# Kernel tuning notes

Measured on AMD Instinct MI355X. Metric: run time of the kernel, lower is better.

The kernel has to match this reference:

```python
import jax, jax.numpy as jnp
import numpy as np

B, N, H, T = 4096, 512, 1024, 10  # batch, input_size, hidden_size, num_iterations
NUM_OPS = 20


def setup_inputs() -> dict:
    key = jax.random.key(0)
    k1, k2, k3, k4 = jax.random.split(key, 4)
    return {
        "x": jax.random.normal(k1, (B, N, 1), jnp.float32),
        "frozen_weight": jax.random.normal(k2, (1, N, H), jnp.float32) / np.sqrt(H),
        "alpha": jax.random.normal(k3, (T, NUM_OPS), jnp.float32),
        "layer_beta": jax.random.normal(k4, (T, 2), jnp.float32),
    }


def _softshrink(x, lam):
    return jnp.where(x > lam, x - lam, jnp.where(x < -lam, x + lam, jnp.zeros_like(x)))


def _hardshrink(x, lam):
    return jnp.where(jnp.abs(x) > lam, x, jnp.zeros_like(x))


def _make_ops(lam):
    # Same 20 ops, same order as the torch ModuleList.
    return [
        lambda x: _softshrink(x, lam),                 # Softshrink(0.001/L)
        jax.nn.relu,                                   # ReLU
        lambda x: x,                                   # Identity
        lambda x: jax.nn.gelu(x, approximate=False),   # GELU (exact erf, torch default)
        jax.nn.elu,                                    # ELU
        lambda x: _hardshrink(x, lam),                 # Hardshrink(0.001/L)
        lambda x: jnp.clip(x, -1.0, 1.0),              # Hardtanh
        jax.nn.hard_swish,                             # Hardswish
        jax.nn.selu,                                   # SELU
        jax.nn.celu,                                   # CELU
        jax.nn.leaky_relu,                             # LeakyReLU (slope 0.01)
        jax.nn.log_sigmoid,                            # LogSigmoid
        lambda x: x - jnp.tanh(x),                     # Tanhshrink
        jax.nn.soft_sign,                              # Softsign
        jax.nn.softplus,                               # Softplus
        jnp.tanh,                                      # Tanh
        jax.nn.sigmoid,                                # Sigmoid
        jax.nn.hard_sigmoid,                           # Hardsigmoid
        jax.nn.silu,                                   # SiLU
        lambda x: x * jnp.tanh(jax.nn.softplus(x)),    # Mish
    ]


def _forward(x, frozen_weight, alpha, layer_beta):
    W = frozen_weight[0]                       # [N, H]
    L = jnp.linalg.norm(W, ord=2) ** 2         # spectral norm squared (Lipschitz)
    lam = 0.001 / L
    ops = _make_ops(lam)

    b = x.shape[0]
    hidden = W.shape[1]
    z = jnp.zeros((b, hidden, 1), dtype=x.dtype)
    z_prev = z
    num_iters = alpha.shape[0]
    for i in range(num_iters):
        aw = jax.nn.softmax(alpha[i])          # [20] (training path, eval_flag=False)
        bw = jax.nn.softmax(layer_beta[i])     # [2]
        # FISTA-style momentum + frozen-weight gradient step
        z_aux = z + (i / (i + 3)) * (z - z_prev)      # [B,H,1]
        Wz = jnp.einsum('nh,bho->bno', W, z_aux)      # [B,N,1]
        grad = jnp.einsum('nh,bno->bho', W, Wz - x)   # [B,H,1]
        z_g = z_aux - grad / L
        # 20-way weighted activation mixture
        z_op = aw[0] * ops[0](z_g)
        for w, op in zip(aw[1:], ops[1:]):
            z_op = z_op + w * op(z_g)
        # beta-weighted residual mix becomes z_prev; z_op becomes current_z
        z_prev = z * bw[0] + z_op * bw[1]
        z = z_op
    return z


def reference(x, frozen_weight, alpha, layer_beta):
    return _forward(x, frozen_weight, alpha, layer_beta)
```

## Files before the change

kernel.cpp:

```cpp
#include <hip/hip_runtime.h>
#include <hip/hip_bf16.h>

#define DI __device__ __forceinline__

typedef float f32x4 __attribute__((ext_vector_type(4)));
typedef __bf16 bf16x8 __attribute__((ext_vector_type(8)));
using bf16_t = __hip_bfloat16;
using ushort_t = unsigned short;

DI void gload_lds16(const void* g, void* l) {
  __builtin_amdgcn_global_load_lds(
      (const __attribute__((address_space(1))) void*)g,
      (__attribute__((address_space(3))) void*)l, 16, 0, 0);
}

DI float rcpf(float x) { return __builtin_amdgcn_rcpf(x); }

DI float act_mix(float x, const float* aw, float lam) {
  const float ax  = fabsf(x);
  const float en  = __expf(-ax);
  const float en2 = en * en;
  const float i1  = rcpf(1.0f + en);
  const float sig = (x >= 0.0f) ? i1 : en * i1;
  const float th  = copysignf((1.0f - en2) * rcpf(1.0f + en2), x);
  const float l1p = __logf(1.0f + en);
  const float sp  = fmaxf(x, 0.0f) + l1p;
  const float lsg = fminf(x, 0.0f) - l1p;
  const float q   = ((x >= 0.0f) ? en2 : 1.0f) * (i1 * i1);
  const float mish = x * (1.0f - q) * rcpf(1.0f + q);
  const float u  = 0.7071067811865476f * x;
  const float au = fabsf(u);
  const float t  = rcpf(1.0f + 0.3275911f * au);
  float poly = fmaf(t, 1.061405429f, -1.453152027f);
  poly = fmaf(t, poly, 1.421413741f);
  poly = fmaf(t, poly, -0.284496736f);
  poly = fmaf(t, poly, 0.254829592f);
  poly *= t;
  const float erfa = 1.0f - poly * __expf(-u * u);
  const float gelu = 0.5f * x * (1.0f + copysignf(erfa, x));
  const float em1  = en - 1.0f;
  const float elu  = (x > 0.0f) ? x : em1;
  const float selu = (x > 0.0f) ? 1.0507009873554805f * x : 1.7580993408473766f * em1;
  const float relu = fmaxf(x, 0.0f);
  const float t6   = fminf(fmaxf(x + 3.0f, 0.0f), 6.0f) * 0.16666666666666666f;
  const float ssh  = (x > lam) ? (x - lam) : ((x < -lam) ? (x + lam) : 0.0f);
  const float hsh  = (ax > lam) ? x : 0.0f;
  const float htan = fminf(fmaxf(x, -1.0f), 1.0f);
  const float lky  = (x >= 0.0f) ? x : 0.01f * x;
  const float ssn  = x * rcpf(1.0f + ax);
  float r = aw[0] * ssh;
  r = fmaf(aw[1],  relu,   r);
  r = fmaf(aw[2],  x,      r);
  r = fmaf(aw[3],  gelu,   r);
  r = fmaf(aw[4],  elu,    r);
  r = fmaf(aw[5],  hsh,    r);
  r = fmaf(aw[6],  htan,   r);
  r = fmaf(aw[7],  x * t6, r);
  r = fmaf(aw[8],  selu,   r);
  r = fmaf(aw[9],  elu,    r);
  r = fmaf(aw[10], lky,    r);
  r = fmaf(aw[11], lsg,    r);
  r = fmaf(aw[12], x - th, r);
  r = fmaf(aw[13], ssn,    r);
  r = fmaf(aw[14], sp,     r);
  r = fmaf(aw[15], th,     r);
  r = fmaf(aw[16], sig,    r);
  r = fmaf(aw[17], t6,     r);
  r = fmaf(aw[18], x * sig, r);
  r = fmaf(aw[19], mish,   r);
  return r;
}

__global__ void k_prep(const float* __restrict__ W, const float* __restrict__ x,
                       bf16_t* __restrict__ Whi, bf16_t* __restrict__ Wlo,
                       bf16_t* __restrict__ Wth, bf16_t* __restrict__ Wtl,
                       bf16_t* __restrict__ xb) {
  int i = blockIdx.x * 256 + threadIdx.x;
  if (i < 512 * 1024) {
    float w = W[i];
    bf16_t h = __float2bfloat16(w);
    bf16_t l = __float2bfloat16(w - __bfloat162float(h));
    Whi[i] = h; Wlo[i] = l;
    int n = i >> 10, hc = i & 1023;
    Wth[hc * 512 + n] = h; Wtl[hc * 512 + n] = l;
  }
  int j = i - 512 * 1024;
  if (j >= 0 && j < 4096 * 512) xb[j] = __float2bfloat16(x[j]);
}

template <int KDIM, bool FIRST, bool WF32>
__global__ __launch_bounds__(256) void k_sqm(
    const bf16_t* __restrict__ Xhi, const bf16_t* __restrict__ Xlo,
    bf16_t* __restrict__ Chi, bf16_t* __restrict__ Clo,
    float* __restrict__ Cf,
    const float* __restrict__ pin, float* __restrict__ pout) {
  __shared__ __align__(16) ushort_t Ah[2][32 * 64], Al[2][32 * 64],
                                    Bh[2][32 * 64], Bl[2][32 * 64];
  __shared__ float red[4];
  const int tid = threadIdx.x, lane = tid & 63, wave = tid >> 6;
  const int wm = wave >> 1, wn = wave & 1;
  const int i0 = blockIdx.x * 32, j0 = blockIdx.y * 32;
  const int bid = blockIdx.y * gridDim.x + blockIdx.x;
  const int r16 = lane & 15, kg = lane >> 4;

  float s = 1.0f;
  if constexpr (!FIRST) {
    float v = pin[tid];
    for (int off = 32; off; off >>= 1) v += __shfl_down(v, off, 64);
    if ((tid & 63) == 0) red[tid >> 6] = v;
    __syncthreads();
    s = 1.0f / (red[0] + red[1] + red[2] + red[3]);
    __syncthreads();
  }

  const int row = tid >> 3;
  const int srcc = (((tid & 7) ^ (row & 7)) << 3);
  const long abase = (long)(i0 + row) * KDIM + srcc;
  const long bbase = (long)(j0 + row) * KDIM + srcc;
  const int ldst = tid * 8;

  auto stage = [&](int buf, int kt) {
    gload_lds16(Xhi + abase + kt, &Ah[buf][ldst]);
    gload_lds16(Xlo + abase + kt, &Al[buf][ldst]);
    gload_lds16(Xhi + bbase + kt, &Bh[buf][ldst]);
    gload_lds16(Xlo + bbase + kt, &Bl[buf][ldst]);
  };

  f32x4 acc = {};
  constexpr int NT = KDIM / 64;
  stage(0, 0);
  __syncthreads();
  for (int t = 0; t < NT; ++t) {
    if (t + 1 < NT) stage((t + 1) & 1, (t + 1) * 64);
    const int b = t & 1;
    const int ra = wm * 16 + r16, rb = wn * 16 + r16;
#pragma unroll
    for (int kk = 0; kk < 64; kk += 32) {
      int oa = ra * 64 + ((kk + kg * 8) ^ ((ra & 7) * 8));
      int ob = rb * 64 + ((kk + kg * 8) ^ ((rb & 7) * 8));
      bf16x8 ah = *(const bf16x8*)&Ah[b][oa];
      bf16x8 al = *(const bf16x8*)&Al[b][oa];
      bf16x8 bh = *(const bf16x8*)&Bh[b][ob];
      bf16x8 bl = *(const bf16x8*)&Bl[b][ob];
      acc = __builtin_amdgcn_mfma_f32_16x16x32_bf16(ah, bh, acc, 0, 0, 0);
      acc = __builtin_amdgcn_mfma_f32_16x16x32_bf16(ah, bl, acc, 0, 0, 0);
      acc = __builtin_amdgcn_mfma_f32_16x16x32_bf16(al, bh, acc, 0, 0, 0);
    }
    __syncthreads();
  }

  float fro = 0.0f;
#pragma unroll
  for (int r = 0; r < 4; ++r) {
    float c = acc[r] * s;
    int orow = i0 + wm * 16 + (lane >> 4) * 4 + r;
    int ocol = j0 + wn * 16 + r16;
    int idx = orow * 512 + ocol;
    bf16_t h = __float2bfloat16(c);
    Chi[idx] = h;
    Clo[idx] = __float2bfloat16(c - __bfloat162float(h));
    if constexpr (WF32) Cf[idx] = c;
    fro = fmaf(c, c, fro);
  }
  for (int off = 32; off; off >>= 1) fro += __shfl_down(fro, off, 64);
  if ((tid & 63) == 0) red[tid >> 6] = fro;
  __syncthreads();
  if (tid == 0) pout[bid] = red[0] + red[1] + red[2] + red[3];
}

__global__ __launch_bounds__(256) void k_G(const bf16_t* __restrict__ Xhi,
                                           const bf16_t* __restrict__ Xlo,
                                           bf16_t* __restrict__ G) {
  __shared__ __align__(16) ushort_t Ah[2][32 * 64], Al[2][32 * 64],
                                    Bh[2][32 * 64], Bl[2][32 * 64];
  const int tid = threadIdx.x, lane = tid & 63, wave = tid >> 6;
  const int wm = wave >> 1, wn = wave & 1;
  const int i0 = blockIdx.x * 32, j0 = blockIdx.y * 32;
  const int r16 = lane & 15, kg = lane >> 4;
  const int row = tid >> 3;
  const int srcc = (((tid & 7) ^ (row & 7)) << 3);
  const long abase = (long)(i0 + row) * 512 + srcc;
  const long bbase = (long)(j0 + row) * 512 + srcc;
  const int ldst = tid * 8;

  auto stage = [&](int buf, int kt) {
    gload_lds16(Xhi + abase + kt, &Ah[buf][ldst]);
    gload_lds16(Xlo + abase + kt, &Al[buf][ldst]);
    gload_lds16(Xhi + bbase + kt, &Bh[buf][ldst]);
    gload_lds16(Xlo + bbase + kt, &Bl[buf][ldst]);
  };

  f32x4 acc = {};
  stage(0, 0);
  __syncthreads();
  for (int t = 0; t < 8; ++t) {
    if (t + 1 < 8) stage((t + 1) & 1, (t + 1) * 64);
    const int b = t & 1;
    const int ra = wm * 16 + r16, rb = wn * 16 + r16;
#pragma unroll
    for (int kk = 0; kk < 64; kk += 32) {
      int oa = ra * 64 + ((kk + kg * 8) ^ ((ra & 7) * 8));
      int ob = rb * 64 + ((kk + kg * 8) ^ ((rb & 7) * 8));
      bf16x8 ah = *(const bf16x8*)&Ah[b][oa];
      bf16x8 al = *(const bf16x8*)&Al[b][oa];
      bf16x8 bh = *(const bf16x8*)&Bh[b][ob];
      bf16x8 bl = *(const bf16x8*)&Bl[b][ob];
      acc = __builtin_amdgcn_mfma_f32_16x16x32_bf16(ah, bh, acc, 0, 0, 0);
      acc = __builtin_amdgcn_mfma_f32_16x16x32_bf16(ah, bl, acc, 0, 0, 0);
      acc = __builtin_amdgcn_mfma_f32_16x16x32_bf16(al, bh, acc, 0, 0, 0);
    }
    __syncthreads();
  }
#pragma unroll
  for (int r = 0; r < 4; ++r) {
    int orow = i0 + wm * 16 + (lane >> 4) * 4 + r;
    int ocol = j0 + wn * 16 + r16;
    G[orow * 1024 + ocol] = __float2bfloat16(acc[r]);
  }
}

__global__ __launch_bounds__(256) void k_dot(const float* __restrict__ A0,
                                             const float* __restrict__ B,
                                             float* __restrict__ numP,
                                             float* __restrict__ denP) {
  __shared__ float redn[4], redd[4];
  const int tid = threadIdx.x;
  const int idx4 = blockIdx.x * 256 + tid;
  const f32x4 a = ((const f32x4*)A0)[idx4];
  const f32x4 b = ((const f32x4*)B)[idx4];
  float nv = a[0]*b[0] + a[1]*b[1] + a[2]*b[2] + a[3]*b[3];
  float dv = 0.0f;
#pragma unroll
  for (int q = 0; q < 4; ++q) {
    int i = idx4 * 4 + q;
    if ((i >> 9) == (i & 511)) dv += b[q];
  }
  for (int off = 32; off; off >>= 1) {
    nv += __shfl_down(nv, off, 64);
    dv += __shfl_down(dv, off, 64);
  }
  if ((tid & 63) == 0) { redn[tid >> 6] = nv; redd[tid >> 6] = dv; }
  __syncthreads();
  if (tid == 0) {
    numP[blockIdx.x] = redn[0] + redn[1] + redn[2] + redn[3];
    denP[blockIdx.x] = redd[0] + redd[1] + redd[2] + redd[3];
  }
}

__global__ __launch_bounds__(256) void k_setup(const float* __restrict__ alpha,
                                               const float* __restrict__ beta,
                                               const float* __restrict__ numP,
                                               const float* __restrict__ denP,
                                               float* __restrict__ params) {
  __shared__ float redn[4], redd[4];
  __shared__ float Lsh;
  const int tid = threadIdx.x;
  float nv = numP[tid], dv = denP[tid];
  for (int off = 32; off; off >>= 1) {
    nv += __shfl_down(nv, off, 64);
    dv += __shfl_down(dv, off, 64);
  }
  if ((tid & 63) == 0) { redn[tid >> 6] = nv; redd[tid >> 6] = dv; }
  __syncthreads();
  if (tid == 0)
    Lsh = (redn[0] + redn[1] + redn[2] + redn[3]) /
          (redd[0] + redd[1] + redd[2] + redd[3]);
  __syncthreads();
  const int t = tid;
  if (t >= 10) return;
  float L = Lsh;
  float invL = 1.0f / L;
  float lam = 0.001f * invL;
  const float* a = alpha + t * 20;
  float mx = a[0];
  for (int k = 1; k < 20; ++k) mx = fmaxf(mx, a[k]);
  float e[20], ssum = 0.0f;
  for (int k = 0; k < 20; ++k) { e[k] = expf(a[k] - mx); ssum += e[k]; }
  float inv = 1.0f / ssum;
  float* P = params + t * 32;
  for (int k = 0; k < 20; ++k) P[k] = e[k] * inv;
  float b0 = beta[t * 2], b1 = beta[t * 2 + 1];
  float bm = fmaxf(b0, b1);
  float eb0 = expf(b0 - bm), eb1 = expf(b1 - bm);
  float bw0 = eb0 / (eb0 + eb1);
  P[20] = ((float)(t + 1) / (float)(t + 4)) * bw0;
  P[21] = invL;
  P[22] = lam;
  P[23] = L;
}

__global__ __launch_bounds__(256, 4) void k_xw(const bf16_t* __restrict__ xb,
                                               const bf16_t* __restrict__ Wth,
                                               const float* __restrict__ prm,
                                               bf16_t* __restrict__ out,
                                               bf16_t* __restrict__ zB,
                                               bf16_t* __restrict__ zaux1) {
  __shared__ __align__(16) ushort_t As[2][64 * 64], Bs[2][64 * 64];
  const int tid = threadIdx.x, lane = tid & 63, wave = tid >> 6;
  const int wm = wave >> 1, wn = wave & 1;
  const int bid = blockIdx.x;
  const int swz = (bid & 7) * 128 + (bid >> 3);
  const int m0 = (swz >> 4) * 64, n0 = (swz & 15) * 64;
  const int r16 = lane & 15, kg = lane >> 4;

  auto stage = [&](int buf, int kt) {
#pragma unroll
    for (int q = 0; q < 2; ++q) {
      int lin = (tid + q * 256) * 8;
      int row = lin >> 6;
      int col = ((((lin >> 3) & 7) ^ (row & 7)) << 3);
      gload_lds16(xb + (long)(m0 + row) * 512 + kt + col, &As[buf][lin]);
      gload_lds16(Wth + (long)(n0 + row) * 512 + kt + col, &Bs[buf][lin]);
    }
  };

  f32x4 acc[2][2] = {};
  auto compute = [&](int b) {
#pragma unroll
    for (int kk = 0; kk < 64; kk += 32) {
      bf16x8 a[2], bb[2];
#pragma unroll
      for (int f = 0; f < 2; ++f) {
        int ra = wm * 32 + f * 16 + r16;
        int rb = wn * 32 + f * 16 + r16;
        a[f]  = *(const bf16x8*)&As[b][ra * 64 + ((kk + kg * 8) ^ ((ra & 7) * 8))];
        bb[f] = *(const bf16x8*)&Bs[b][rb * 64 + ((kk + kg * 8) ^ ((rb & 7) * 8))];
      }
#pragma unroll
      for (int i = 0; i < 2; ++i)
#pragma unroll
        for (int j = 0; j < 2; ++j)
          acc[i][j] = __builtin_amdgcn_mfma_f32_16x16x32_bf16(a[i], bb[j], acc[i][j], 0, 0, 0);
    }
  };

  stage(0, 0);
  stage(1, 64);
  asm volatile("s_waitcnt vmcnt(4)" ::: "memory");
  __builtin_amdgcn_s_barrier();
  __builtin_amdgcn_sched_barrier(0);

  for (int t = 0; t < 8; ++t) {
    compute(t & 1);
    if (t == 7) break;
    asm volatile("s_waitcnt lgkmcnt(0)" ::: "memory");
    __builtin_amdgcn_sched_barrier(0);
    __builtin_amdgcn_s_barrier();
    if (t + 2 < 8) {
      stage(t & 1, (t + 2) * 64);
      asm volatile("s_waitcnt vmcnt(4)" ::: "memory");
    } else {
      asm volatile("s_waitcnt vmcnt(0)" ::: "memory");
    }
    __builtin_amdgcn_s_barrier();
    __builtin_amdgcn_sched_barrier(0);
  }
  __builtin_amdgcn_sched_barrier(0);

  const float invL = prm[21];
  const float d0 = prm[20];
  const float lam = prm[22];
  float aw[20];
#pragma unroll
  for (int k = 0; k < 20; ++k) aw[k] = prm[k];
#pragma unroll
  for (int i = 0; i < 2; ++i)
#pragma unroll
    for (int j = 0; j < 2; ++j)
#pragma unroll
      for (int r = 0; r < 4; ++r) {
        int row = m0 + wm * 32 + i * 16 + (lane >> 4) * 4 + r;
        int col = n0 + wn * 32 + j * 16 + r16;
        long idx = (long)row * 1024 + col;
        bf16_t xv = __float2bfloat16(acc[i][j][r] * invL);
        out[idx] = xv;
        float zop = act_mix(__bfloat162float(xv), aw, lam);
        zB[idx] = __float2bfloat16(zop);
        zaux1[idx] = __float2bfloat16(zop * (1.0f + d0));
      }
}

template <bool LAST>
__global__ __launch_bounds__(256, 4) void k_iter(const bf16_t* __restrict__ A,
                                                 const bf16_t* __restrict__ G,
                                                 const bf16_t* __restrict__ xWs,
                                                 bf16_t* __restrict__ zauxN,
                                                 bf16_t* zB, float* zio,
                                                 const float* __restrict__ prm) {
  __shared__ __align__(16) ushort_t As[2][64 * 64], Bs[2][64 * 64];
  const int tid = threadIdx.x, lane = tid & 63, wave = tid >> 6;
  const int wm = wave >> 1, wn = wave & 1;
  const int bid = blockIdx.x;
  const int swz = (bid & 7) * 128 + (bid >> 3);
  const int m0 = (swz >> 4) * 64, n0 = (swz & 15) * 64;
  const int r16 = lane & 15, kg = lane >> 4;

  auto stage = [&](int buf, int kt) {
#pragma unroll
    for (int q = 0; q < 2; ++q) {
      int lin = (tid + q * 256) * 8;
      int row = lin >> 6;
      int col = ((((lin >> 3) & 7) ^ (row & 7)) << 3);
      gload_lds16(A + (long)(m0 + row) * 1024 + kt + col, &As[buf][lin]);
      gload_lds16(G + (long)(n0 + row) * 1024 + kt + col, &Bs[buf][lin]);
    }
  };

  f32x4 acc[2][2] = {};
  auto compute = [&](int b) {
#pragma unroll
    for (int kk = 0; kk < 64; kk += 32) {
      bf16x8 a[2], bb[2];
#pragma unroll
      for (int f = 0; f < 2; ++f) {
        int ra = wm * 32 + f * 16 + r16;
        int rb = wn * 32 + f * 16 + r16;
        a[f]  = *(const bf16x8*)&As[b][ra * 64 + ((kk + kg * 8) ^ ((ra & 7) * 8))];
        bb[f] = *(const bf16x8*)&Bs[b][rb * 64 + ((kk + kg * 8) ^ ((rb & 7) * 8))];
      }
#pragma unroll
      for (int i = 0; i < 2; ++i)
#pragma unroll
        for (int j = 0; j < 2; ++j)
          acc[i][j] = __builtin_amdgcn_mfma_f32_16x16x32_bf16(a[i], bb[j], acc[i][j], 0, 0, 0);
    }
  };

  stage(0, 0);
  stage(1, 64);
  asm volatile("s_waitcnt vmcnt(4)" ::: "memory");
  __builtin_amdgcn_s_barrier();
  __builtin_amdgcn_sched_barrier(0);

  for (int t = 0; t < 16; ++t) {
    compute(t & 1);
    if (t == 15) break;
    asm volatile("s_waitcnt lgkmcnt(0)" ::: "memory");
    __builtin_amdgcn_sched_barrier(0);
    __builtin_amdgcn_s_barrier();
    if (t + 2 < 16) {
      stage(t & 1, (t + 2) * 64);
      asm volatile("s_waitcnt vmcnt(4)" ::: "memory");
    } else {
      asm volatile("s_waitcnt vmcnt(0)" ::: "memory");
    }
    __builtin_amdgcn_s_barrier();
    __builtin_amdgcn_sched_barrier(0);
  }
  __builtin_amdgcn_sched_barrier(0);

  const float d_i = prm[20];
  const float invL = prm[21];
  const float lam = prm[22];
  float aw[20];
#pragma unroll
  for (int k = 0; k < 20; ++k) aw[k] = prm[k];

  float xv[2][2][4], av[2][2][4], zv[2][2][4];
#pragma unroll
  for (int i = 0; i < 2; ++i)
#pragma unroll
    for (int j = 0; j < 2; ++j)
#pragma unroll
      for (int r = 0; r < 4; ++r) {
        int row = m0 + wm * 32 + i * 16 + (lane >> 4) * 4 + r;
        int col = n0 + wn * 32 + j * 16 + r16;
        long idx = (long)row * 1024 + col;
        xv[i][j][r] = __bfloat162float(xWs[idx]);
        av[i][j][r] = __bfloat162float(A[idx]);
        if (!LAST) zv[i][j][r] = __bfloat162float(zB[idx]);
      }
#pragma unroll
  for (int i = 0; i < 2; ++i)
#pragma unroll
    for (int j = 0; j < 2; ++j)
#pragma unroll
      for (int r = 0; r < 4; ++r) {
        int row = m0 + wm * 32 + i * 16 + (lane >> 4) * 4 + r;
        int col = n0 + wn * 32 + j * 16 + r16;
        long idx = (long)row * 1024 + col;
        float zg = fmaf(-acc[i][j][r], invL, av[i][j][r] + xv[i][j][r]);
        float zop = act_mix(zg, aw, lam);
        if (LAST) {
          zio[idx] = zop;
        } else {
          zB[idx] = __float2bfloat16(zop);
          zauxN[idx] = __float2bfloat16(fmaf(d_i, zop - zv[i][j][r], zop));
        }
      }
}

extern "C" void kernel_launch(void* const* d_in, const int* in_sizes, int n_in,
                              void* d_out, int out_size, void* d_ws, size_t ws_size,
                              hipStream_t stream) {
  const float* x     = (const float*)d_in[0];
  const float* W     = (const float*)d_in[1];
  const float* alpha = (const float*)d_in[2];
  const float* beta  = (const float*)d_in[3];
  float* zout = (float*)d_out;

  char* ws = (char*)d_ws;
  const size_t MB = 1u << 20;
  float* pb[11];
  for (int k = 0; k < 11; ++k) pb[k] = (float*)(ws + (size_t)k * 1024);
  float* numP   = (float*)(ws + 12 * 1024);
  float* denP   = (float*)(ws + 13 * 1024);
  float* params = (float*)(ws + 14 * 1024);
  const size_t HDR = 32768;
  float*  A0f  = (float*)(ws + HDR);
  float*  Bf   = (float*)(ws + HDR + 1 * MB);
  bf16_t* H0   = (bf16_t*)(ws + HDR + 2 * MB);
  bf16_t* L0   = (bf16_t*)(ws + HDR + 2 * MB + 512 * 1024);
  bf16_t* H1   = (bf16_t*)(ws + HDR + 3 * MB);
  bf16_t* L1   = (bf16_t*)(ws + HDR + 3 * MB + 512 * 1024);
  bf16_t* Whi  = (bf16_t*)(ws + HDR + 4 * MB);
  bf16_t* Wlo  = (bf16_t*)(ws + HDR + 5 * MB);
  bf16_t* Wth  = (bf16_t*)(ws + HDR + 6 * MB);
  bf16_t* Wtl  = (bf16_t*)(ws + HDR + 7 * MB);
  bf16_t* Gm   = (bf16_t*)(ws + HDR + 8 * MB);
  bf16_t* xb   = (bf16_t*)(ws + HDR + 10 * MB);
  bf16_t* xWs  = (bf16_t*)(ws + HDR + 18 * MB);
  bf16_t* zx0  = (bf16_t*)(ws + HDR + 26 * MB);
  bf16_t* zx1  = (bf16_t*)(ws + HDR + 34 * MB);
  bf16_t* zB   = (bf16_t*)(ws + HDR + 42 * MB);

  k_prep<<<10240, 256, 0, stream>>>(W, x, Whi, Wlo, Wth, Wtl, xb);

  k_sqm<1024, true, true><<<dim3(16, 16), 256, 0, stream>>>(
      Whi, Wlo, H0, L0, A0f, nullptr, pb[0]);
  bf16_t* Hs[2] = {H0, H1};
  bf16_t* Ls[2] = {L0, L1};
  int pp = 0;
  for (int k = 0; k < 9; ++k) {
    if (k == 8)
      k_sqm<512, false, true><<<dim3(16, 16), 256, 0, stream>>>(
          Hs[pp], Ls[pp], Hs[pp ^ 1], Ls[pp ^ 1], Bf, pb[k], pb[k + 1]);
    else
      k_sqm<512, false, false><<<dim3(16, 16), 256, 0, stream>>>(
          Hs[pp], Ls[pp], Hs[pp ^ 1], Ls[pp ^ 1], nullptr, pb[k], pb[k + 1]);
    pp ^= 1;
  }
  k_dot<<<256, 256, 0, stream>>>(A0f, Bf, numP, denP);
  k_setup<<<1, 256, 0, stream>>>(alpha, beta, numP, denP, params);

  k_G<<<dim3(32, 32), 256, 0, stream>>>(Wth, Wtl, Gm);
  k_xw<<<1024, 256, 0, stream>>>(xb, Wth, params, xWs, zB, zx1);

  bf16_t* zx[2] = {zx0, zx1};
  for (int i = 1; i < 9; ++i)
    k_iter<false><<<1024, 256, 0, stream>>>(zx[i & 1], Gm, xWs, zx[(i + 1) & 1],
                                            zB, zout, params + i * 32);
  k_iter<true><<<1024, 256, 0, stream>>>(zx[9 & 1], Gm, xWs, zx0 ,
                                         zB, zout, params + 9 * 32);
}
```

Before: 369.1 us.

## Fuse spectral-norm dot into squaring, merge G/xW launches, reuse LDS tiles in iterations

```diff
diff --git a/kernel.cpp b/kernel.cpp
--- a/kernel.cpp
+++ b/kernel.cpp
@@ -15,6 +15,12 @@
 }
 
 DI float rcpf(float x) { return __builtin_amdgcn_rcpf(x); }
+
+DI float us2f(ushort_t u) {
+  bf16_t h;
+  *reinterpret_cast<ushort_t*>(&h) = u;
+  return __bfloat162float(h);
+}
 
 DI float act_mix(float x, const float* aw, float lam) {
   const float ax  = fabsf(x);
@@ -88,15 +94,16 @@
   if (j >= 0 && j < 4096 * 512) xb[j] = __float2bfloat16(x[j]);
 }
 
-template <int KDIM, bool FIRST, bool WF32>
+template <int KDIM, bool FIRST, bool DOT>
 __global__ __launch_bounds__(256) void k_sqm(
     const bf16_t* __restrict__ Xhi, const bf16_t* __restrict__ Xlo,
     bf16_t* __restrict__ Chi, bf16_t* __restrict__ Clo,
     float* __restrict__ Cf,
-    const float* __restrict__ pin, float* __restrict__ pout) {
+    const float* __restrict__ pin, float* __restrict__ pout,
+    float* __restrict__ numP, float* __restrict__ denP) {
   __shared__ __align__(16) ushort_t Ah[2][32 * 64], Al[2][32 * 64],
                                     Bh[2][32 * 64], Bl[2][32 * 64];
-  __shared__ float red[4];
+  __shared__ float red[4], redd[4];
   const int tid = threadIdx.x, lane = tid & 63, wave = tid >> 6;
   const int wm = wave >> 1, wn = wave & 1;
   const int i0 = blockIdx.x * 32, j0 = blockIdx.y * 32;
@@ -149,101 +156,37 @@
     __syncthreads();
   }
 
-  float fro = 0.0f;
+  float fro = 0.0f, dvp = 0.0f;
 #pragma unroll
   for (int r = 0; r < 4; ++r) {
     float c = acc[r] * s;
     int orow = i0 + wm * 16 + (lane >> 4) * 4 + r;
     int ocol = j0 + wn * 16 + r16;
     int idx = orow * 512 + ocol;
-    bf16_t h = __float2bfloat16(c);
-    Chi[idx] = h;
-    Clo[idx] = __float2bfloat16(c - __bfloat162float(h));
-    if constexpr (WF32) Cf[idx] = c;
-    fro = fmaf(c, c, fro);
-  }
-  for (int off = 32; off; off >>= 1) fro += __shfl_down(fro, off, 64);
-  if ((tid & 63) == 0) red[tid >> 6] = fro;
-  __syncthreads();
-  if (tid == 0) pout[bid] = red[0] + red[1] + red[2] + red[3];
-}
-
-__global__ __launch_bounds__(256) void k_G(const bf16_t* __restrict__ Xhi,
-                                           const bf16_t* __restrict__ Xlo,
-                                           bf16_t* __restrict__ G) {
-  __shared__ __align__(16) ushort_t Ah[2][32 * 64], Al[2][32 * 64],
-                                    Bh[2][32 * 64], Bl[2][32 * 64];
-  const int tid = threadIdx.x, lane = tid & 63, wave = tid >> 6;
-  const int wm = wave >> 1, wn = wave & 1;
-  const int i0 = blockIdx.x * 32, j0 = blockIdx.y * 32;
-  const int r16 = lane & 15, kg = lane >> 4;
-  const int row = tid >> 3;
-  const int srcc = (((tid & 7) ^ (row & 7)) << 3);
-  const long abase = (long)(i0 + row) * 512 + srcc;
-  const long bbase = (long)(j0 + row) * 512 + srcc;
-  const int ldst = tid * 8;
-
-  auto stage = [&](int buf, int kt) {
-    gload_lds16(Xhi + abase + kt, &Ah[buf][ldst]);
-    gload_lds16(Xlo + abase + kt, &Al[buf][ldst]);
-    gload_lds16(Xhi + bbase + kt, &Bh[buf][ldst]);
-    gload_lds16(Xlo + bbase + kt, &Bl[buf][ldst]);
-  };
-
-  f32x4 acc = {};
-  stage(0, 0);
-  __syncthreads();
-  for (int t = 0; t < 8; ++t) {
-    if (t + 1 < 8) stage((t + 1) & 1, (t + 1) * 64);
-    const int b = t & 1;
-    const int ra = wm * 16 + r16, rb = wn * 16 + r16;
-#pragma unroll
-    for (int kk = 0; kk < 64; kk += 32) {
-      int oa = ra * 64 + ((kk + kg * 8) ^ ((ra & 7) * 8));
-      int ob = rb * 64 + ((kk + kg * 8) ^ ((rb & 7) * 8));
-      bf16x8 ah = *(const bf16x8*)&Ah[b][oa];
-      bf16x8 al = *(const bf16x8*)&Al[b][oa];
-      bf16x8 bh = *(const bf16x8*)&Bh[b][ob];
-      bf16x8 bl = *(const bf16x8*)&Bl[b][ob];
-      acc = __builtin_amdgcn_mfma_f32_16x16x32_bf16(ah, bh, acc, 0, 0, 0);
-      acc = __builtin_amdgcn_mfma_f32_16x16x32_bf16(ah, bl, acc, 0, 0, 0);
-      acc = __builtin_amdgcn_mfma_f32_16x16x32_bf16(al, bh, acc, 0, 0, 0);
-    }
-    __syncthreads();
-  }
-#pragma unroll
-  for (int r = 0; r < 4; ++r) {
-    int orow = i0 + wm * 16 + (lane >> 4) * 4 + r;
-    int ocol = j0 + wn * 16 + r16;
-    G[orow * 1024 + ocol] = __float2bfloat16(acc[r]);
-  }
-}
-
-__global__ __launch_bounds__(256) void k_dot(const float* __restrict__ A0,
-                                             const float* __restrict__ B,
-                                             float* __restrict__ numP,
-                                             float* __restrict__ denP) {
-  __shared__ float redn[4], redd[4];
-  const int tid = threadIdx.x;
-  const int idx4 = blockIdx.x * 256 + tid;
-  const f32x4 a = ((const f32x4*)A0)[idx4];
-  const f32x4 b = ((const f32x4*)B)[idx4];
-  float nv = a[0]*b[0] + a[1]*b[1] + a[2]*b[2] + a[3]*b[3];
-  float dv = 0.0f;
-#pragma unroll
-  for (int q = 0; q < 4; ++q) {
-    int i = idx4 * 4 + q;
-    if ((i >> 9) == (i & 511)) dv += b[q];
+    if constexpr (DOT) {
+      fro = fmaf(Cf[idx], c, fro);
+      if (orow == ocol) dvp += c;
+    } else {
+      bf16_t h = __float2bfloat16(c);
+      Chi[idx] = h;
+      Clo[idx] = __float2bfloat16(c - __bfloat162float(h));
+      if constexpr (FIRST) Cf[idx] = c;
+      fro = fmaf(c, c, fro);
+    }
   }
   for (int off = 32; off; off >>= 1) {
-    nv += __shfl_down(nv, off, 64);
-    dv += __shfl_down(dv, off, 64);
-  }
-  if ((tid & 63) == 0) { redn[tid >> 6] = nv; redd[tid >> 6] = dv; }
+    fro += __shfl_down(fro, off, 64);
+    if constexpr (DOT) dvp += __shfl_down(dvp, off, 64);
+  }
+  if ((tid & 63) == 0) { red[tid >> 6] = fro; if constexpr (DOT) redd[tid >> 6] = dvp; }
   __syncthreads();
   if (tid == 0) {
-    numP[blockIdx.x] = redn[0] + redn[1] + redn[2] + redn[3];
-    denP[blockIdx.x] = redd[0] + redd[1] + redd[2] + redd[3];
+    if constexpr (DOT) {
+      numP[bid] = red[0] + red[1] + red[2] + red[3];
+      denP[bid] = redd[0] + redd[1] + redd[2] + redd[3];
+    } else {
+      pout[bid] = red[0] + red[1] + red[2] + red[3];
+    }
   }
 }
 
@@ -289,19 +232,69 @@
   P[23] = L;
 }
 
-__global__ __launch_bounds__(256, 4) void k_xw(const bf16_t* __restrict__ xb,
-                                               const bf16_t* __restrict__ Wth,
-                                               const float* __restrict__ prm,
-                                               bf16_t* __restrict__ out,
-                                               bf16_t* __restrict__ zB,
-                                               bf16_t* __restrict__ zaux1) {
-  __shared__ __align__(16) ushort_t As[2][64 * 64], Bs[2][64 * 64];
+__global__ __launch_bounds__(256, 4) void k_gx(
+    const bf16_t* __restrict__ xb, const bf16_t* __restrict__ Wth,
+    const bf16_t* __restrict__ Wtl, const float* __restrict__ prm,
+    bf16_t* __restrict__ Gm, bf16_t* __restrict__ xWs,
+    bf16_t* __restrict__ zB, bf16_t* __restrict__ zaux1) {
+  __shared__ __align__(16) ushort_t smem[16384];
   const int tid = threadIdx.x, lane = tid & 63, wave = tid >> 6;
   const int wm = wave >> 1, wn = wave & 1;
+  const int r16 = lane & 15, kg = lane >> 4;
+
+  if ((int)blockIdx.x >= 1024) {
+    const int gb = blockIdx.x - 1024;
+    const int i0 = (gb & 31) * 32, j0 = (gb >> 5) * 32;
+    ushort_t* Ah = smem;
+    ushort_t* Al = smem + 4096;
+    ushort_t* Bh = smem + 8192;
+    ushort_t* Bl = smem + 12288;
+    const int row = tid >> 3;
+    const int srcc = (((tid & 7) ^ (row & 7)) << 3);
+    const long abase = (long)(i0 + row) * 512 + srcc;
+    const long bbase = (long)(j0 + row) * 512 + srcc;
+    const int ldst = tid * 8;
+    auto stg = [&](int buf, int kt) {
+      gload_lds16(Wth + abase + kt, &Ah[buf * 2048 + ldst]);
+      gload_lds16(Wtl + abase + kt, &Al[buf * 2048 + ldst]);
+      gload_lds16(Wth + bbase + kt, &Bh[buf * 2048 + ldst]);
+      gload_lds16(Wtl + bbase + kt, &Bl[buf * 2048 + ldst]);
+    };
+    f32x4 acc = {};
+    stg(0, 0);
+    __syncthreads();
+    for (int t = 0; t < 8; ++t) {
+      if (t + 1 < 8) stg((t + 1) & 1, (t + 1) * 64);
+      const int b = t & 1;
+      const int ra = wm * 16 + r16, rb = wn * 16 + r16;
+#pragma unroll
+      for (int kk = 0; kk < 64; kk += 32) {
+        int oa = b * 2048 + ra * 64 + ((kk + kg * 8) ^ ((ra & 7) * 8));
+        int ob = b * 2048 + rb * 64 + ((kk + kg * 8) ^ ((rb & 7) * 8));
+        bf16x8 ah = *(const bf16x8*)&Ah[oa];
+        bf16x8 al = *(const bf16x8*)&Al[oa];
+        bf16x8 bh = *(const bf16x8*)&Bh[ob];
+        bf16x8 bl = *(const bf16x8*)&Bl[ob];
+        acc = __builtin_amdgcn_mfma_f32_16x16x32_bf16(ah, bh, acc, 0, 0, 0);
+        acc = __builtin_amdgcn_mfma_f32_16x16x32_bf16(ah, bl, acc, 0, 0, 0);
+        acc = __builtin_amdgcn_mfma_f32_16x16x32_bf16(al, bh, acc, 0, 0, 0);
+      }
+      __syncthreads();
+    }
+#pragma unroll
+    for (int r = 0; r < 4; ++r) {
+      int orow = i0 + wm * 16 + (lane >> 4) * 4 + r;
+      int ocol = j0 + wn * 16 + r16;
+      Gm[orow * 1024 + ocol] = __float2bfloat16(acc[r]);
+    }
+    return;
+  }
+
   const int bid = blockIdx.x;
   const int swz = (bid & 7) * 128 + (bid >> 3);
   const int m0 = (swz >> 4) * 64, n0 = (swz & 15) * 64;
-  const int r16 = lane & 15, kg = lane >> 4;
+  ushort_t* As = smem;
+  ushort_t* Bs = smem + 8192;
 
   auto stage = [&](int buf, int kt) {
 #pragma unroll
@@ -309,8 +302,8 @@
       int lin = (tid + q * 256) * 8;
       int row = lin >> 6;
       int col = ((((lin >> 3) & 7) ^ (row & 7)) << 3);
-      gload_lds16(xb + (long)(m0 + row) * 512 + kt + col, &As[buf][lin]);
-      gload_lds16(Wth + (long)(n0 + row) * 512 + kt + col, &Bs[buf][lin]);
+      gload_lds16(xb + (long)(m0 + row) * 512 + kt + col, &As[buf * 4096 + lin]);
+      gload_lds16(Wth + (long)(n0 + row) * 512 + kt + col, &Bs[buf * 4096 + lin]);
     }
   };
 
@@ -323,8 +316,8 @@
       for (int f = 0; f < 2; ++f) {
         int ra = wm * 32 + f * 16 + r16;
         int rb = wn * 32 + f * 16 + r16;
-        a[f]  = *(const bf16x8*)&As[b][ra * 64 + ((kk + kg * 8) ^ ((ra & 7) * 8))];
-        bb[f] = *(const bf16x8*)&Bs[b][rb * 64 + ((kk + kg * 8) ^ ((rb & 7) * 8))];
+        a[f]  = *(const bf16x8*)&As[b * 4096 + ra * 64 + ((kk + kg * 8) ^ ((ra & 7) * 8))];
+        bb[f] = *(const bf16x8*)&Bs[b * 4096 + rb * 64 + ((kk + kg * 8) ^ ((rb & 7) * 8))];
       }
 #pragma unroll
       for (int i = 0; i < 2; ++i)
@@ -373,7 +366,7 @@
         int col = n0 + wn * 32 + j * 16 + r16;
         long idx = (long)row * 1024 + col;
         bf16_t xv = __float2bfloat16(acc[i][j][r] * invL);
-        out[idx] = xv;
+        xWs[idx] = xv;
         float zop = act_mix(__bfloat162float(xv), aw, lam);
         zB[idx] = __float2bfloat16(zop);
         zaux1[idx] = __float2bfloat16(zop * (1.0f + d0));
@@ -395,6 +388,13 @@
   const int m0 = (swz >> 4) * 64, n0 = (swz & 15) * 64;
   const int r16 = lane & 15, kg = lane >> 4;
 
+  const float d_i = prm[20];
+  const float invL = prm[21];
+  const float lam = prm[22];
+  float aw[20];
+#pragma unroll
+  for (int k = 0; k < 20; ++k) aw[k] = prm[k];
+
   auto stage = [&](int buf, int kt) {
 #pragma unroll
     for (int q = 0; q < 2; ++q) {
@@ -426,6 +426,9 @@
     }
   };
 
+  const int snap_t = n0 >> 6;
+  ushort_t ar[2][2][4], xr[2][2][4], zr[2][2][4];
+
   stage(0, 0);
   stage(1, 64);
   asm volatile("s_waitcnt vmcnt(4)" ::: "memory");
@@ -434,13 +437,46 @@
 
   for (int t = 0; t < 16; ++t) {
     compute(t & 1);
+    if (t == snap_t) {
+#pragma unroll
+      for (int i = 0; i < 2; ++i)
+#pragma unroll
+        for (int j = 0; j < 2; ++j)
+#pragma unroll
+          for (int r = 0; r < 4; ++r) {
+            int rl = wm * 32 + i * 16 + (lane >> 4) * 4 + r;
+            int cl = wn * 32 + j * 16 + r16;
+            ar[i][j][r] = As[t & 1][rl * 64 + (cl ^ ((rl & 7) * 8))];
+          }
+    }
+    if (t == 13) {
+#pragma unroll
+      for (int i = 0; i < 2; ++i)
+#pragma unroll
+        for (int j = 0; j < 2; ++j)
+#pragma unroll
+          for (int r = 0; r < 4; ++r) {
+            int row = m0 + wm * 32 + i * 16 + (lane >> 4) * 4 + r;
+            int col = n0 + wn * 32 + j * 16 + r16;
+            long idx = (long)row * 1024 + col;
+            xr[i][j][r] = *reinterpret_cast<const ushort_t*>(&xWs[idx]);
+            if (!LAST) zr[i][j][r] = *reinterpret_cast<const ushort_t*>(&zB[idx]);
+          }
+    }
     if (t == 15) break;
     asm volatile("s_waitcnt lgkmcnt(0)" ::: "memory");
     __builtin_amdgcn_sched_barrier(0);
     __builtin_amdgcn_s_barrier();
     if (t + 2 < 16) {
       stage(t & 1, (t + 2) * 64);
-      asm volatile("s_waitcnt vmcnt(4)" ::: "memory");
+      if (t == 13) {
+        if constexpr (LAST)
+          asm volatile("s_waitcnt vmcnt(20)" ::: "memory");
+        else
+          asm volatile("s_waitcnt vmcnt(36)" ::: "memory");
+      } else {
+        asm volatile("s_waitcnt vmcnt(4)" ::: "memory");
+      }
     } else {
       asm volatile("s_waitcnt vmcnt(0)" ::: "memory");
     }
@@ -449,14 +485,6 @@
   }
   __builtin_amdgcn_sched_barrier(0);
 
-  const float d_i = prm[20];
-  const float invL = prm[21];
-  const float lam = prm[22];
-  float aw[20];
-#pragma unroll
-  for (int k = 0; k < 20; ++k) aw[k] = prm[k];
-
-  float xv[2][2][4], av[2][2][4], zv[2][2][4];
 #pragma unroll
   for (int i = 0; i < 2; ++i)
 #pragma unroll
@@ -466,26 +494,13 @@
         int row = m0 + wm * 32 + i * 16 + (lane >> 4) * 4 + r;
         int col = n0 + wn * 32 + j * 16 + r16;
         long idx = (long)row * 1024 + col;
-        xv[i][j][r] = __bfloat162float(xWs[idx]);
-        av[i][j][r] = __bfloat162float(A[idx]);
-        if (!LAST) zv[i][j][r] = __bfloat162float(zB[idx]);
-      }
-#pragma unroll
-  for (int i = 0; i < 2; ++i)
-#pragma unroll
-    for (int j = 0; j < 2; ++j)
-#pragma unroll
-      for (int r = 0; r < 4; ++r) {
-        int row = m0 + wm * 32 + i * 16 + (lane >> 4) * 4 + r;
-        int col = n0 + wn * 32 + j * 16 + r16;
-        long idx = (long)row * 1024 + col;
-        float zg = fmaf(-acc[i][j][r], invL, av[i][j][r] + xv[i][j][r]);
+        float zg = fmaf(-acc[i][j][r], invL, us2f(ar[i][j][r]) + us2f(xr[i][j][r]));
         float zop = act_mix(zg, aw, lam);
         if (LAST) {
           zio[idx] = zop;
         } else {
           zB[idx] = __float2bfloat16(zop);
-          zauxN[idx] = __float2bfloat16(fmaf(d_i, zop - zv[i][j][r], zop));
+          zauxN[idx] = __float2bfloat16(fmaf(d_i, zop - us2f(zr[i][j][r]), zop));
         }
       }
 }
@@ -501,14 +516,13 @@
 
   char* ws = (char*)d_ws;
   const size_t MB = 1u << 20;
-  float* pb[11];
-  for (int k = 0; k < 11; ++k) pb[k] = (float*)(ws + (size_t)k * 1024);
-  float* numP   = (float*)(ws + 12 * 1024);
-  float* denP   = (float*)(ws + 13 * 1024);
-  float* params = (float*)(ws + 14 * 1024);
+  float* pb[9];
+  for (int k = 0; k < 9; ++k) pb[k] = (float*)(ws + (size_t)k * 1024);
+  float* numP   = (float*)(ws + 10 * 1024);
+  float* denP   = (float*)(ws + 11 * 1024);
+  float* params = (float*)(ws + 12 * 1024);
   const size_t HDR = 32768;
   float*  A0f  = (float*)(ws + HDR);
-  float*  Bf   = (float*)(ws + HDR + 1 * MB);
   bf16_t* H0   = (bf16_t*)(ws + HDR + 2 * MB);
   bf16_t* L0   = (bf16_t*)(ws + HDR + 2 * MB + 512 * 1024);
   bf16_t* H1   = (bf16_t*)(ws + HDR + 3 * MB);
@@ -526,25 +540,22 @@
 
   k_prep<<<10240, 256, 0, stream>>>(W, x, Whi, Wlo, Wth, Wtl, xb);
 
-  k_sqm<1024, true, true><<<dim3(16, 16), 256, 0, stream>>>(
-      Whi, Wlo, H0, L0, A0f, nullptr, pb[0]);
+  k_sqm<1024, true, false><<<dim3(16, 16), 256, 0, stream>>>(
+      Whi, Wlo, H0, L0, A0f, nullptr, pb[0], nullptr, nullptr);
   bf16_t* Hs[2] = {H0, H1};
   bf16_t* Ls[2] = {L0, L1};
   int pp = 0;
-  for (int k = 0; k < 9; ++k) {
-    if (k == 8)
-      k_sqm<512, false, true><<<dim3(16, 16), 256, 0, stream>>>(
-          Hs[pp], Ls[pp], Hs[pp ^ 1], Ls[pp ^ 1], Bf, pb[k], pb[k + 1]);
-    else
-      k_sqm<512, false, false><<<dim3(16, 16), 256, 0, stream>>>(
-          Hs[pp], Ls[pp], Hs[pp ^ 1], Ls[pp ^ 1], nullptr, pb[k], pb[k + 1]);
+  for (int k = 0; k < 7; ++k) {
+    k_sqm<512, false, false><<<dim3(16, 16), 256, 0, stream>>>(
+        Hs[pp], Ls[pp], Hs[pp ^ 1], Ls[pp ^ 1], nullptr, pb[k], pb[k + 1],
+        nullptr, nullptr);
     pp ^= 1;
   }
-  k_dot<<<256, 256, 0, stream>>>(A0f, Bf, numP, denP);
+  k_sqm<512, false, true><<<dim3(16, 16), 256, 0, stream>>>(
+      Hs[pp], Ls[pp], nullptr, nullptr, A0f, pb[7], nullptr, numP, denP);
   k_setup<<<1, 256, 0, stream>>>(alpha, beta, numP, denP, params);
 
-  k_G<<<dim3(32, 32), 256, 0, stream>>>(Wth, Wtl, Gm);
-  k_xw<<<1024, 256, 0, stream>>>(xb, Wth, params, xWs, zB, zx1);
+  k_gx<<<2048, 256, 0, stream>>>(xb, Wth, Wtl, params, Gm, xWs, zB, zx1);
 
   bf16_t* zx[2] = {zx0, zx1};
   for (int i = 1; i < 9; ++i)
```

Measured after the change: 422.2 us. 1.14x slower.
